# Optimization experiments

Measured on AMD Instinct MI355X. Metric: run time of the kernel, lower is better.

## Reference

```python
import jax, jax.numpy as jnp
import numpy as np

C = 768
H = 12
T = 4096
B = 1
EPS = 1e-5


def setup_inputs() -> dict:
    key = jax.random.key(0)
    ks = jax.random.split(key, 16)
    s = 0.02
    return {
        "x": jax.random.normal(ks[0], (B, T, C), jnp.float32),
        "ln1_w": jnp.ones((C,), jnp.float32),
        "ln1_b": jnp.zeros((C,), jnp.float32),
        "W_attn": jax.random.normal(ks[1], (C, 3 * C), jnp.float32) * s,
        "b_attn": jnp.zeros((3 * C,), jnp.float32),
        "W_proj": jax.random.normal(ks[2], (C, C), jnp.float32) * s,
        "b_proj": jnp.zeros((C,), jnp.float32),
        "ln2_w": jnp.ones((C,), jnp.float32),
        "ln2_b": jnp.zeros((C,), jnp.float32),
        "W_fc": jax.random.normal(ks[3], (C, 4 * C), jnp.float32) * s,
        "b_fc": jnp.zeros((4 * C,), jnp.float32),
        "W_fc2": jax.random.normal(ks[4], (4 * C, C), jnp.float32) * s,
        "b_fc2": jnp.zeros((C,), jnp.float32),
    }


def _layernorm(x, w, b):
    mu = jnp.mean(x, axis=-1, keepdims=True)
    var = jnp.var(x, axis=-1, keepdims=True)
    return (x - mu) * jax.lax.rsqrt(var + EPS) * w + b


def _attn(x, W_attn, b_attn, W_proj, b_proj):
    Bb, Tt, Cc = x.shape
    hd = Cc // H
    qkv = x @ W_attn + b_attn                       # (B,T,3C)
    q, k, v = jnp.split(qkv, 3, axis=-1)
    q = q.reshape(Bb, Tt, H, hd).transpose(0, 2, 1, 3)  # (B,H,T,hd)
    k = k.reshape(Bb, Tt, H, hd).transpose(0, 2, 1, 3)
    v = v.reshape(Bb, Tt, H, hd).transpose(0, 2, 1, 3)
    att = jnp.einsum('bhqd,bhkd->bhqk', q, k) * (1.0 / np.sqrt(hd))
    causal = jnp.tril(jnp.ones((Tt, Tt), bool))
    att = jnp.where(causal, att, -jnp.inf)
    att = jax.nn.softmax(att, axis=-1)
    y = jnp.einsum('bhqk,bhkd->bhqd', att, v)       # (B,H,T,hd)
    y = y.transpose(0, 2, 1, 3).reshape(Bb, Tt, Cc)
    return y @ W_proj + b_proj


def _mlp(x, W_fc, b_fc, W_fc2, b_fc2):
    h = jax.nn.gelu(x @ W_fc + b_fc, approximate=False)
    return h @ W_fc2 + b_fc2


def reference(x, ln1_w, ln1_b, W_attn, b_attn, W_proj, b_proj,
              ln2_w, ln2_b, W_fc, b_fc, W_fc2, b_fc2):
    x = x + _attn(_layernorm(x, ln1_w, ln1_b), W_attn, b_attn, W_proj, b_proj)
    x = x + _mlp(_layernorm(x, ln2_w, ln2_b), W_fc, b_fc, W_fc2, b_fc2)
    return x
```

## Files before the change

kernel.cpp:

```cpp
#include <hip/hip_runtime.h>
#include <hip/hip_bf16.h>
#include <math.h>
#include <type_traits>

#define TSEQ 4096
#define CDIM 768
#define NH 12
#define HD 64

typedef float f32x4 __attribute__((ext_vector_type(4)));
typedef __bf16 bf16x8 __attribute__((ext_vector_type(8)));
typedef short s16x8 __attribute__((ext_vector_type(8)));
typedef uint u32x4 __attribute__((ext_vector_type(4)));

__device__ inline ushort f2bf(float f) {
  __hip_bfloat16 h = __float2bfloat16(f);
  return __builtin_bit_cast(ushort, h);
}

__device__ inline void async16(const void* g, void* l) {
  __builtin_amdgcn_global_load_lds(
      (__attribute__((address_space(1))) unsigned int*)(uintptr_t)g,
      (__attribute__((address_space(3))) unsigned int*)(uintptr_t)l, 16, 0, 0);
}

__device__ inline float exp2_fast(float x) {
  float r;
  asm volatile("v_exp_f32 %0, %1\n\ts_nop 0" : "=v"(r) : "v"(x));
  return r;
}

__device__ inline uint cvtpk(float a, float b) {
  uint r;
  asm volatile("v_cvt_pk_bf16_f32 %0, %1, %2" : "=v"(r) : "v"(a), "v"(b));
  return r;
}

__device__ inline bf16x8 frag_read(const ushort* base, int row, int kk, int lane) {
  const int byte = row * 128 + ((((kk * 4 + (lane >> 4)) ^ (row & 7))) << 4);
  return *(const bf16x8*)((const char*)base + byte);
}

__global__ __launch_bounds__(256) void wconv_t(
    const float* __restrict__ W, ushort* __restrict__ Wt, int K, int N)
{
  __shared__ float sm[32][33];
  const int n0 = blockIdx.x * 32, k0 = blockIdx.y * 32;
  const int c = threadIdx.x & 31, r0 = threadIdx.x >> 5;
#pragma unroll
  for (int i = 0; i < 4; ++i) {
    const int r = r0 + i * 8;
    sm[r][c] = W[(size_t)(k0 + r) * N + n0 + c];
  }
  __syncthreads();
#pragma unroll
  for (int i = 0; i < 4; ++i) {
    const int r = r0 + i * 8;
    Wt[(size_t)(n0 + r) * K + k0 + c] = f2bf(sm[c][r]);
  }
}

__global__ __launch_bounds__(256) void ln_kernel(
    const float* __restrict__ x, const float* __restrict__ w,
    const float* __restrict__ b, ushort* __restrict__ out)
{
  const int row = blockIdx.x;
  const int tid = threadIdx.x;
  const float* xr = x + (size_t)row * CDIM;
  float v[3];
  float s1 = 0.f, s2 = 0.f;
#pragma unroll
  for (int i = 0; i < 3; ++i) {
    v[i] = xr[tid + i * 256];
    s1 += v[i];
    s2 += v[i] * v[i];
  }
#pragma unroll
  for (int off = 32; off >= 1; off >>= 1) {
    s1 += __shfl_xor(s1, off, 64);
    s2 += __shfl_xor(s2, off, 64);
  }
  __shared__ float red1[4], red2[4];
  if ((tid & 63) == 0) { red1[tid >> 6] = s1; red2[tid >> 6] = s2; }
  __syncthreads();
  s1 = red1[0] + red1[1] + red1[2] + red1[3];
  s2 = red2[0] + red2[1] + red2[2] + red2[3];
  const float mu = s1 * (1.f / CDIM);
  const float var = s2 * (1.f / CDIM) - mu * mu;
  const float inv = rsqrtf(var + 1e-5f);
#pragma unroll
  for (int i = 0; i < 3; ++i) {
    const int c = tid + i * 256;
    out[(size_t)row * CDIM + c] = f2bf((v[i] - mu) * inv * w[c] + b[c]);
  }
}

template <int EPI, int BN>
__global__ __launch_bounds__(256) void gemm_bt(
    const ushort* __restrict__ A, const ushort* __restrict__ Bt,
    const float* __restrict__ bias, const float* __restrict__ res,
    ushort* __restrict__ outb, float* __restrict__ outf,
    int M, int N, int K, int gx)
{
  constexpr int NW = BN / 32;
  __shared__ __align__(16) ushort As[3][128 * 32];
  __shared__ __align__(16) ushort Bs[3][BN * 32];
  const int tid = threadIdx.x;
  const int lane = tid & 63;
  const int wv = tid >> 6;
  const int nwg = (int)gridDim.x;
  const int bid = (int)blockIdx.x;
  const int sw = (bid & 7) * (nwg >> 3) + (bid >> 3);
  const int rowBase = (sw / gx) * 128;
  const int colBase = (sw % gx) * BN;
  const int wr = (wv >> 1) * 64;
  const int wc = (wv & 1) * (BN / 2);

  f32x4 acc[4][NW] = {};

  const int e0 = tid * 8;
  const int r0 = e0 >> 5, c0 = e0 & 31;
  const int e1 = (tid + 256) * 8;
  const int r1 = e1 >> 5, c1 = e1 & 31;

  const ushort* Ag0 = A + (size_t)(rowBase + r0) * K + c0;
  const ushort* Ag1 = A + (size_t)(rowBase + r1) * K + c1;
  const ushort* Bg0 = Bt + (size_t)(colBase + r0) * K + c0;
  const ushort* Bg1 = Bt + (size_t)(colBase + r1) * K + c1;

  auto stage = [&](int buf, int k0) {
    async16(Ag0 + k0, &As[buf][e0]);
    async16(Ag1 + k0, &As[buf][e1]);
    async16(Bg0 + k0, &Bs[buf][e0]);
    if (BN == 128) async16(Bg1 + k0, &Bs[buf][e1]);
  };

  const int nt = K / 32;
  stage(0, 0);
  stage(1, 32);
  int b0 = 0, b1 = 1, b2 = 2;
  for (int t = 0; t < nt; ++t) {
    if (t < nt - 1) {
      if (BN == 128) asm volatile("s_waitcnt vmcnt(4)" ::: "memory");
      else           asm volatile("s_waitcnt vmcnt(3)" ::: "memory");
    } else {
      asm volatile("s_waitcnt vmcnt(0)" ::: "memory");
    }
    __builtin_amdgcn_sched_barrier(0);
    __builtin_amdgcn_s_barrier();
    __builtin_amdgcn_sched_barrier(0);
    if (t + 2 < nt) stage(b2, t * 32 + 64);

    bf16x8 af[4], bfr[NW];
#pragma unroll
    for (int m = 0; m < 4; ++m)
      af[m] = *(const bf16x8*)&As[b0][(wr + m * 16 + (lane & 15)) * 32 + (lane >> 4) * 8];
#pragma unroll
    for (int n = 0; n < NW; ++n)
      bfr[n] = *(const bf16x8*)&Bs[b0][(wc + n * 16 + (lane & 15)) * 32 + (lane >> 4) * 8];
    __builtin_amdgcn_s_setprio(1);
#pragma unroll
    for (int m = 0; m < 4; ++m)
#pragma unroll
      for (int n = 0; n < NW; ++n)
        acc[m][n] = __builtin_amdgcn_mfma_f32_16x16x32_bf16(af[m], bfr[n], acc[m][n], 0, 0, 0);
    __builtin_amdgcn_s_setprio(0);
    const int tmp = b0; b0 = b1; b1 = b2; b2 = tmp;
  }

#pragma unroll
  for (int n = 0; n < NW; ++n) {
    const int gc = colBase + wc + n * 16 + (lane & 15);
    const float bv = bias[gc];
#pragma unroll
    for (int m = 0; m < 4; ++m) {
#pragma unroll
      for (int j = 0; j < 4; ++j) {
        const int gr = rowBase + wr + m * 16 + (lane >> 4) * 4 + j;
        const float v = acc[m][n][j] + bv;
        if (EPI == 0) {
          outb[(size_t)gr * N + gc] = f2bf(v);
        } else if (EPI == 1) {
          outf[(size_t)gr * N + gc] = res[(size_t)gr * N + gc] + v;
        } else {
          const float g = 0.5f * v * (1.0f + erff(v * 0.70710678118654752f));
          outb[(size_t)gr * N + gc] = f2bf(g);
        }
      }
    }
  }
}

__global__ __launch_bounds__(256) void attn_kernel(
    const ushort* __restrict__ qkv, ushort* __restrict__ att)
{
  __shared__ __align__(16) ushort Ks[2][64 * 64];
  __shared__ __align__(16) ushort Vt[2][64 * 64];

  const int tid = threadIdx.x;
  const int lane = tid & 63;
  const int wv = tid >> 6;
  const int g = lane >> 4;
  const int ql = lane & 15;
  const int p_ = blockIdx.x & 255, grp = blockIdx.x >> 8;
  const int item = (grp & 1) ? (grp * 256 + 255 - p_) : (grp * 256 + p_);
  const int qb = 63 - (item / 12);
  const int h = item % 12;
  const int t0 = qb * 64;
  const size_t rs = 3 * CDIM;
  const int qo = h * HD, ko = CDIM + h * HD, vo = 2 * CDIM + h * HD;

  const float cexp = 0.18033688f;
  const float cbias = -32.0f * 0.18033688f;

  const int L0 = tid * 16, L1 = (tid + 256) * 16;
  const int r_0 = L0 >> 7, c_0 = ((L0 >> 4) & 7) ^ (r_0 & 7);
  const int r_1 = L1 >> 7, c_1 = ((L1 >> 4) & 7) ^ (r_1 & 7);
  const ushort* kg0 = qkv + (size_t)r_0 * rs + ko + c_0 * 8;
  const ushort* kg1 = qkv + (size_t)r_1 * rs + ko + c_1 * 8;

  const int vt = (tid >> 3) * 2;
  const int vd = (tid & 7) * 8;
  const int slot2 = (32 * ((vt >> 4) >> 1) + 8 * ((vt >> 2) & 3) +
                     4 * ((vt >> 4) & 1) + (vt & 3)) * 2;
  const ushort* vg = qkv + (size_t)vt * rs + vo + vd;

  const ushort* qrow = qkv + (size_t)(t0 + wv * 16 + ql) * rs + qo + g * 8;
  const bf16x8 aq0 = *(const bf16x8*)(qrow);
  const bf16x8 aq1 = *(const bf16x8*)(qrow + 32);

  s16x8 vA0 = *(const s16x8*)(vg);
  s16x8 vA1 = *(const s16x8*)(vg + rs);
  async16(kg0, (char*)Ks[0] + L0);
  async16(kg1, (char*)Ks[0] + L1);
#pragma unroll
  for (int jj = 0; jj < 8; ++jj) {
    const int d = vd + jj;
    const uint val = (uint)(ushort)vA0[jj] | ((uint)(ushort)vA1[jj] << 16);
    *(uint*)((char*)Vt[0] + d * 128 + (slot2 ^ (((d >> 1) & 7) << 4))) = val;
  }

  f32x4 accO[4] = {};
  f32x4 accL = {};
  const bf16x8 ones = __builtin_bit_cast(bf16x8,
      (u32x4){0x3F803F80u, 0x3F803F80u, 0x3F803F80u, 0x3F803F80u});
  const int swzv = (ql >> 1) & 7;

  int cur = 0;
  auto body = [&](int kb, int curb, auto diag_c) {
    constexpr bool DIAG = decltype(diag_c)::value;
    const size_t koff = (size_t)(kb + 1) * 64 * rs;

    if (!DIAG) {
      vA0 = *(const s16x8*)(vg + koff);
      vA1 = *(const s16x8*)(vg + koff + rs);
      asm volatile("s_waitcnt vmcnt(2) lgkmcnt(0)" ::: "memory");
    } else {
      asm volatile("s_waitcnt vmcnt(0) lgkmcnt(0)" ::: "memory");
    }
    __builtin_amdgcn_sched_barrier(0);
    __builtin_amdgcn_s_barrier();
    __builtin_amdgcn_sched_barrier(0);

    if (!DIAG) {
      async16(kg0 + koff, (char*)Ks[curb ^ 1] + L0);
      async16(kg1 + koff, (char*)Ks[curb ^ 1] + L1);
    }

    f32x4 accS[4] = {};
    __builtin_amdgcn_s_setprio(1);
#pragma unroll
    for (int kk = 0; kk < 2; ++kk) {
      const bf16x8 a_q = kk ? aq1 : aq0;
#pragma unroll
      for (int n = 0; n < 4; ++n)
        accS[n] = __builtin_amdgcn_mfma_f32_16x16x32_bf16(
            frag_read(Ks[curb], n * 16 + ql, kk, lane), a_q, accS[n], 0, 0, 0);
    }
    __builtin_amdgcn_s_setprio(0);

    uint pk[8];
#pragma unroll
    for (int n = 0; n < 4; ++n) {
      float pv[4];
#pragma unroll
      for (int j = 0; j < 4; ++j) {
        float s = exp2_fast(fmaf(accS[n][j], cexp, cbias));
        if (DIAG && (16 * n + 4 * g + j) > (wv * 16 + ql)) s = 0.f;
        pv[j] = s;
      }
      pk[2 * n] = cvtpk(pv[0], pv[1]);
      pk[2 * n + 1] = cvtpk(pv[2], pv[3]);
    }
    const bf16x8 pf0 = __builtin_bit_cast(bf16x8, (u32x4){pk[0], pk[1], pk[2], pk[3]});
    const bf16x8 pf1 = __builtin_bit_cast(bf16x8, (u32x4){pk[4], pk[5], pk[6], pk[7]});

    __builtin_amdgcn_s_setprio(1);
#pragma unroll
    for (int kk = 0; kk < 2; ++kk) {
      const bf16x8 a_p = kk ? pf1 : pf0;
#pragma unroll
      for (int n = 0; n < 4; ++n) {
        const int byte = (n * 16 + ql) * 128 + ((kk * 64 + g * 16) ^ (swzv << 4));
        const bf16x8 bv = *(const bf16x8*)((const char*)Vt[curb] + byte);
        accO[n] = __builtin_amdgcn_mfma_f32_16x16x32_bf16(a_p, bv, accO[n], 0, 0, 0);
      }
      accL = __builtin_amdgcn_mfma_f32_16x16x32_bf16(a_p, ones, accL, 0, 0, 0);
    }
    __builtin_amdgcn_s_setprio(0);

    if (!DIAG) {
#pragma unroll
      for (int jj = 0; jj < 8; ++jj) {
        const int d = vd + jj;
        const uint val = (uint)(ushort)vA0[jj] | ((uint)(ushort)vA1[jj] << 16);
        *(uint*)((char*)Vt[curb ^ 1] + d * 128 + (slot2 ^ (((d >> 1) & 7) << 4))) = val;
      }
    }
  };

  for (int kb = 0; kb < qb; ++kb) {
    body(kb, cur, std::false_type{});
    cur ^= 1;
  }
  body(qb, cur, std::true_type{});

  float inv[4];
#pragma unroll
  for (int jr = 0; jr < 4; ++jr) inv[jr] = 1.0f / accL[jr];
#pragma unroll
  for (int n = 0; n < 4; ++n)
#pragma unroll
    for (int jr = 0; jr < 4; ++jr) {
      const int tq = t0 + wv * 16 + 4 * g + jr;
      const int d = n * 16 + ql;
      att[(size_t)tq * CDIM + h * HD + d] = f2bf(accO[n][jr] * inv[jr]);
    }
}

extern "C" void kernel_launch(void* const* d_in, const int* in_sizes, int n_in,
                              void* d_out, int out_size, void* d_ws, size_t ws_size,
                              hipStream_t stream)
{
  const float* x      = (const float*)d_in[0];
  const float* ln1_w  = (const float*)d_in[1];
  const float* ln1_b  = (const float*)d_in[2];
  const float* W_attn = (const float*)d_in[3];
  const float* b_attn = (const float*)d_in[4];
  const float* W_proj = (const float*)d_in[5];
  const float* b_proj = (const float*)d_in[6];
  const float* ln2_w  = (const float*)d_in[7];
  const float* ln2_b  = (const float*)d_in[8];
  const float* W_fc   = (const float*)d_in[9];
  const float* b_fc   = (const float*)d_in[10];
  const float* W_fc2  = (const float*)d_in[11];
  const float* b_fc2  = (const float*)d_in[12];
  float* out = (float*)d_out;

  char* base = (char*)d_ws;
  size_t off = 0;
  auto alloc = [&](size_t bytes) -> void* {
    void* q = base + off;
    off = (off + bytes + 255) & ~(size_t)255;
    return q;
  };
  ushort* Wt_attn = (ushort*)alloc(768ull * 2304 * 2);
  ushort* Wt_proj = (ushort*)alloc(768ull * 768 * 2);
  ushort* Wt_fc   = (ushort*)alloc(768ull * 3072 * 2);
  ushort* Wt_fc2  = (ushort*)alloc(3072ull * 768 * 2);
  ushort* t_ln    = (ushort*)alloc(4096ull * 768 * 2);
  ushort* t_att   = (ushort*)alloc(4096ull * 768 * 2);
  float*  t_x1    = (float*) alloc(4096ull * 768 * 4);
  ushort* t_big   = (ushort*)alloc(4096ull * 3072 * 2);
  ushort* t_qkv = t_big;
  ushort* t_h   = t_big;

  wconv_t<<<dim3(2304 / 32, 768 / 32), 256, 0, stream>>>(W_attn, Wt_attn, 768, 2304);
  wconv_t<<<dim3(768 / 32, 768 / 32), 256, 0, stream>>>(W_proj, Wt_proj, 768, 768);
  wconv_t<<<dim3(3072 / 32, 768 / 32), 256, 0, stream>>>(W_fc, Wt_fc, 768, 3072);
  wconv_t<<<dim3(768 / 32, 3072 / 32), 256, 0, stream>>>(W_fc2, Wt_fc2, 3072, 768);

  ln_kernel<<<4096, 256, 0, stream>>>(x, ln1_w, ln1_b, t_ln);
  gemm_bt<0, 128><<<18 * 32, 256, 0, stream>>>(
      t_ln, Wt_attn, b_attn, nullptr, t_qkv, nullptr, 4096, 2304, 768, 18);
  attn_kernel<<<dim3(768), 256, 0, stream>>>(t_qkv, t_att);
  gemm_bt<1, 64><<<12 * 32, 256, 0, stream>>>(
      t_att, Wt_proj, b_proj, x, nullptr, t_x1, 4096, 768, 768, 12);
  ln_kernel<<<4096, 256, 0, stream>>>(t_x1, ln2_w, ln2_b, t_ln);
  gemm_bt<2, 128><<<24 * 32, 256, 0, stream>>>(
      t_ln, Wt_fc, b_fc, nullptr, t_h, nullptr, 4096, 3072, 768, 24);
  gemm_bt<1, 64><<<12 * 32, 256, 0, stream>>>(
      t_h, Wt_fc2, b_fc2, t_x1, nullptr, out, 4096, 768, 3072, 12);
}
```

Baseline: 198.5 us.

## Split attention work across waves by query and key halves with LDS reduction

Each wave previously handled 16 query rows against all 64 keys of a block. Now the four waves form a 2x2 grid: each covers 32 query rows against 32 keys. Each K and V fragment read from LDS then feeds two MFMAs, which roughly halves LDS fragment traffic per MFMA. The cost is doubled Q registers and accumulators, a V-transpose layout change, and an end-of-kernel LDS reduction of the partial O and L sums between key-half wave pairs, with extra barriers.

```diff
diff --git a/kernel.cpp b/kernel.cpp
--- a/kernel.cpp
+++ b/kernel.cpp
@@ -202,6 +202,8 @@
   const int wv = tid >> 6;
   const int g = lane >> 4;
   const int ql = lane & 15;
+  const int kh = wv & 1;
+  const int qh = wv >> 1;
   const int p_ = blockIdx.x & 255, grp = blockIdx.x >> 8;
   const int item = (grp & 1) ? (grp * 256 + 255 - p_) : (grp * 256 + p_);
   const int qb = 63 - (item / 12);
@@ -221,13 +223,17 @@
 
   const int vt = (tid >> 3) * 2;
   const int vd = (tid & 7) * 8;
-  const int slot2 = (32 * ((vt >> 4) >> 1) + 8 * ((vt >> 2) & 3) +
-                     4 * ((vt >> 4) & 1) + (vt & 3)) * 2;
+  const int s32 = vt & 31;
+  const int col2 = (vt >> 5) * 64 + (8 * ((s32 >> 2) & 3) + 4 * (s32 >> 4) + (s32 & 3)) * 2;
   const ushort* vg = qkv + (size_t)vt * rs + vo + vd;
 
-  const ushort* qrow = qkv + (size_t)(t0 + wv * 16 + ql) * rs + qo + g * 8;
-  const bf16x8 aq0 = *(const bf16x8*)(qrow);
-  const bf16x8 aq1 = *(const bf16x8*)(qrow + 32);
+  bf16x8 qf[2][2];
+#pragma unroll
+  for (int qg = 0; qg < 2; ++qg) {
+    const ushort* qrow = qkv + (size_t)(t0 + 32 * qh + 16 * qg + ql) * rs + qo + g * 8;
+    qf[qg][0] = *(const bf16x8*)(qrow);
+    qf[qg][1] = *(const bf16x8*)(qrow + 32);
+  }
 
   s16x8 vA0 = *(const s16x8*)(vg);
   s16x8 vA1 = *(const s16x8*)(vg + rs);
@@ -237,11 +243,11 @@
   for (int jj = 0; jj < 8; ++jj) {
     const int d = vd + jj;
     const uint val = (uint)(ushort)vA0[jj] | ((uint)(ushort)vA1[jj] << 16);
-    *(uint*)((char*)Vt[0] + d * 128 + (slot2 ^ (((d >> 1) & 7) << 4))) = val;
-  }
-
-  f32x4 accO[4] = {};
-  f32x4 accL = {};
+    *(uint*)((char*)Vt[0] + d * 128 + (col2 ^ (((d >> 1) & 7) << 4))) = val;
+  }
+
+  f32x4 accO[2][4] = {};
+  f32x4 accL[2] = {};
   const bf16x8 ones = __builtin_bit_cast(bf16x8,
       (u32x4){0x3F803F80u, 0x3F803F80u, 0x3F803F80u, 0x3F803F80u});
   const int swzv = (ql >> 1) & 7;
@@ -267,46 +273,51 @@
       async16(kg1 + koff, (char*)Ks[curb ^ 1] + L1);
     }
 
-    f32x4 accS[4] = {};
+    f32x4 accS[2][2] = {};
     __builtin_amdgcn_s_setprio(1);
 #pragma unroll
-    for (int kk = 0; kk < 2; ++kk) {
-      const bf16x8 a_q = kk ? aq1 : aq0;
-#pragma unroll
-      for (int n = 0; n < 4; ++n)
-        accS[n] = __builtin_amdgcn_mfma_f32_16x16x32_bf16(
-            frag_read(Ks[curb], n * 16 + ql, kk, lane), a_q, accS[n], 0, 0, 0);
-    }
+    for (int kg = 0; kg < 2; ++kg)
+#pragma unroll
+      for (int kk = 0; kk < 2; ++kk) {
+        const bf16x8 A = frag_read(Ks[curb], 32 * kh + 16 * kg + ql, kk, lane);
+#pragma unroll
+        for (int qg = 0; qg < 2; ++qg)
+          accS[kg][qg] = __builtin_amdgcn_mfma_f32_16x16x32_bf16(
+              A, qf[qg][kk], accS[kg][qg], 0, 0, 0);
+      }
     __builtin_amdgcn_s_setprio(0);
 
-    uint pk[8];
+    bf16x8 pa[2];
+#pragma unroll
+    for (int qg = 0; qg < 2; ++qg) {
+      float e[2][4];
+#pragma unroll
+      for (int kg = 0; kg < 2; ++kg)
+#pragma unroll
+        for (int j = 0; j < 4; ++j) {
+          float s = exp2_fast(fmaf(accS[kg][qg][j], cexp, cbias));
+          if (DIAG && (32 * kh + 16 * kg + 4 * g + j) > (32 * qh + 16 * qg + ql)) s = 0.f;
+          e[kg][j] = s;
+        }
+      const uint w0 = cvtpk(e[0][0], e[0][1]);
+      const uint w1 = cvtpk(e[0][2], e[0][3]);
+      const uint w2 = cvtpk(e[1][0], e[1][1]);
+      const uint w3 = cvtpk(e[1][2], e[1][3]);
+      pa[qg] = __builtin_bit_cast(bf16x8, (u32x4){w0, w1, w2, w3});
+    }
+
+    __builtin_amdgcn_s_setprio(1);
 #pragma unroll
     for (int n = 0; n < 4; ++n) {
-      float pv[4];
-#pragma unroll
-      for (int j = 0; j < 4; ++j) {
-        float s = exp2_fast(fmaf(accS[n][j], cexp, cbias));
-        if (DIAG && (16 * n + 4 * g + j) > (wv * 16 + ql)) s = 0.f;
-        pv[j] = s;
-      }
-      pk[2 * n] = cvtpk(pv[0], pv[1]);
-      pk[2 * n + 1] = cvtpk(pv[2], pv[3]);
-    }
-    const bf16x8 pf0 = __builtin_bit_cast(bf16x8, (u32x4){pk[0], pk[1], pk[2], pk[3]});
-    const bf16x8 pf1 = __builtin_bit_cast(bf16x8, (u32x4){pk[4], pk[5], pk[6], pk[7]});
-
-    __builtin_amdgcn_s_setprio(1);
-#pragma unroll
-    for (int kk = 0; kk < 2; ++kk) {
-      const bf16x8 a_p = kk ? pf1 : pf0;
-#pragma unroll
-      for (int n = 0; n < 4; ++n) {
-        const int byte = (n * 16 + ql) * 128 + ((kk * 64 + g * 16) ^ (swzv << 4));
-        const bf16x8 bv = *(const bf16x8*)((const char*)Vt[curb] + byte);
-        accO[n] = __builtin_amdgcn_mfma_f32_16x16x32_bf16(a_p, bv, accO[n], 0, 0, 0);
-      }
-      accL = __builtin_amdgcn_mfma_f32_16x16x32_bf16(a_p, ones, accL, 0, 0, 0);
-    }
+      const int byte = (16 * n + ql) * 128 + ((kh * 64 + 16 * g) ^ (swzv << 4));
+      const bf16x8 bv = *(const bf16x8*)((const char*)Vt[curb] + byte);
+#pragma unroll
+      for (int qg = 0; qg < 2; ++qg)
+        accO[qg][n] = __builtin_amdgcn_mfma_f32_16x16x32_bf16(pa[qg], bv, accO[qg][n], 0, 0, 0);
+    }
+#pragma unroll
+    for (int qg = 0; qg < 2; ++qg)
+      accL[qg] = __builtin_amdgcn_mfma_f32_16x16x32_bf16(pa[qg], ones, accL[qg], 0, 0, 0);
     __builtin_amdgcn_s_setprio(0);
 
     if (!DIAG) {
@@ -314,7 +325,7 @@
       for (int jj = 0; jj < 8; ++jj) {
         const int d = vd + jj;
         const uint val = (uint)(ushort)vA0[jj] | ((uint)(ushort)vA1[jj] << 16);
-        *(uint*)((char*)Vt[curb ^ 1] + d * 128 + (slot2 ^ (((d >> 1) & 7) << 4))) = val;
+        *(uint*)((char*)Vt[curb ^ 1] + d * 128 + (col2 ^ (((d >> 1) & 7) << 4))) = val;
       }
     }
   };
@@ -325,17 +336,39 @@
   }
   body(qb, cur, std::true_type{});
 
-  float inv[4];
-#pragma unroll
-  for (int jr = 0; jr < 4; ++jr) inv[jr] = 1.0f / accL[jr];
-#pragma unroll
-  for (int n = 0; n < 4; ++n)
-#pragma unroll
-    for (int jr = 0; jr < 4; ++jr) {
-      const int tq = t0 + wv * 16 + 4 * g + jr;
-      const int d = n * 16 + ql;
-      att[(size_t)tq * CDIM + h * HD + d] = f2bf(accO[n][jr] * inv[jr]);
-    }
+  __syncthreads();
+  float* mO = (float*)&Ks[0][0];
+  float* mL = (float*)&Vt[0][0];
+  if (kh == 1) {
+#pragma unroll
+    for (int qg = 0; qg < 2; ++qg) {
+#pragma unroll
+      for (int n = 0; n < 4; ++n)
+        *(f32x4*)&mO[(((qh * 2 + qg) * 4 + n) * 64 + lane) * 4] = accO[qg][n];
+      *(f32x4*)&mL[((qh * 2 + qg) * 64 + lane) * 4] = accL[qg];
+    }
+  }
+  __syncthreads();
+  if (kh == 0) {
+#pragma unroll
+    for (int qg = 0; qg < 2; ++qg) {
+      const f32x4 ls = accL[qg] + *(const f32x4*)&mL[((qh * 2 + qg) * 64 + lane) * 4];
+      f32x4 inv4;
+#pragma unroll
+      for (int jr = 0; jr < 4; ++jr) inv4[jr] = 1.0f / ls[jr];
+#pragma unroll
+      for (int n = 0; n < 4; ++n) {
+        const f32x4 o = accO[qg][n] +
+            *(const f32x4*)&mO[(((qh * 2 + qg) * 4 + n) * 64 + lane) * 4];
+#pragma unroll
+        for (int jr = 0; jr < 4; ++jr) {
+          const int tq = t0 + 32 * qh + 16 * qg + 4 * g + jr;
+          const int d = 16 * n + ql;
+          att[(size_t)tq * CDIM + h * HD + d] = f2bf(o[jr] * inv4[jr]);
+        }
+      }
+    }
+  }
 }
 
 extern "C" void kernel_launch(void* const* d_in, const int* in_sizes, int n_in,
```

Measured after the change: 194.7 us. No clear change (-1.9%).
